# Kernel optimization log

Measured on AMD Instinct MI355X. Metric: run time of the kernel, lower is better.

Reference implementation:

```python
import jax, jax.numpy as jnp
import numpy as np

EPS = 1e-10


def _log_scaling(feats):
    """Raw feats (..., 15): xmin,ymin,xmax,ymax,area,angle,pca_big,pca_small,hu1..hu7
    -> (..., 17): xmin..area, log|pca_big..hu7|, lshape, cosangle, sinangle."""
    lshape = jnp.sqrt(feats[..., 7:8]) / (jnp.sqrt(feats[..., 6:7]) + EPS)
    cosangle = jnp.cos(feats[..., 5:6])
    sinangle = jnp.sin(feats[..., 5:6])
    logged = jnp.log(jnp.abs(feats[..., 5:]) + EPS)  # cols 5..14 logged
    # original drops the (logged) angle column 5 and keeps logged cols 6..14
    return jnp.concatenate([feats[..., :5], logged[..., 1:], lshape, cosangle, sinangle], axis=-1)


def _make_parents(n_trees, P, seed=0):
    """Valid topologically-ordered tree: parent[p] < p, parent[0] = 0 (root)."""
    rng = np.random.default_rng(seed)
    idx = np.arange(P)
    high = np.maximum(idx, 1)
    par = rng.integers(0, 2**31 - 1, size=(n_trees, P)) % high[None, :]
    par[:, 0] = 0
    return par.astype(np.int32)


def setup_inputs() -> dict:
    key = jax.random.key(0)
    k1, k2, k3, k4 = jax.random.split(key, 4)
    B, N, H, W = 2, 2, 1024, 1024
    P = H * W
    x = jax.random.normal(k1, (B, N, H, W), dtype=jnp.float32) * 10.0
    weight = jax.random.uniform(k2, (N, 17, 1), dtype=jnp.float32, minval=-0.01, maxval=0.01)
    bias = jnp.zeros((N, 1), dtype=jnp.float32)
    attrs = jax.random.uniform(k3, (B, N, P, 15), dtype=jnp.float32) * 4.0
    parents = jnp.asarray(_make_parents(B * N, P).reshape(B, N, P))
    return {"x": x, "weight": weight, "bias": bias, "attrs": attrs, "parents": parents}


def _path_sum(contrib_pad, par_pad, P):
    """Pointer-doubling root-to-node path sums over a tree with sentinel at index P."""
    iters = max(int(np.ceil(np.log2(max(P, 2)))), 1)

    def body(i, carry):
        v, p = carry
        return v + v[p], p[p]

    v, _ = jax.lax.fori_loop(0, iters, body, (contrib_pad, par_pad))
    return v[:P]


def reference(x, weight, bias, attrs, parents):
    B, N, H, W = x.shape
    P = H * W
    xf = x.reshape(B, N, P)
    idx = jnp.arange(P, dtype=parents.dtype)
    is_root = parents == idx  # (B,N,P)
    parent_vals = jnp.take_along_axis(xf, parents, axis=-1)
    diff = jnp.where(is_root, xf, xf - parent_vals)  # per-node gray-level increment
    feats = _log_scaling(attrs)  # (B,N,P,17)
    lin = jnp.einsum('bnpf,nfo->bnpo', feats, weight) + bias[None, :, None, :]
    scores = jax.nn.sigmoid(lin[..., 0])  # (B,N,P)
    contrib = diff * scores
    # sentinel node P with contribution 0; roots point at the sentinel
    sent = jnp.full((B, N, 1), P, dtype=parents.dtype)
    par_pad = jnp.concatenate([jnp.where(is_root, P, parents), sent], axis=-1)
    contrib_pad = jnp.concatenate([contrib, jnp.zeros((B, N, 1), x.dtype)], axis=-1)
    out = jax.vmap(jax.vmap(lambda c, p: _path_sum(c, p, P)))(contrib_pad, par_pad)
    return out.reshape(B, N, H, W)
```

## Files before the change

kernel.cpp:

```cpp
#include <hip/hip_runtime.h>
#include <math.h>

#define EPSF 1e-10f
#define P_NODES (1 << 20)
#define T_FRONT 65536
#define T_MID   262144

struct __align__(8) NodePair {
    float v;
    int   par;
};

__global__ __launch_bounds__(256) void score_kernel(
    const float* __restrict__ x,
    const float* __restrict__ weight,
    const float* __restrict__ bias,
    const float* __restrict__ attrs,
    const int*   __restrict__ parents,
    NodePair*    __restrict__ dst,
    int N)
{
    __shared__ float sA[256 * 15];

    const int t = threadIdx.x;
    const int blockBase = blockIdx.x * 256;
    const int idx = blockBase + t;

    const float4* ab4 = (const float4*)(attrs + (size_t)blockBase * 15);
    float4* sA4 = (float4*)sA;
#pragma unroll
    for (int k = t; k < 960; k += 256)
        sA4[k] = ab4[k];

    const int tree = blockBase >> 20;
    const int n    = tree % N;
    const float* w = weight + n * 17;
    const float  b = bias[n];

    __syncthreads();

    const float* a = &sA[t * 15];

    float acc = b;
    acc += a[0] * w[0];
    acc += a[1] * w[1];
    acc += a[2] * w[2];
    acc += a[3] * w[3];
    acc += a[4] * w[4];

    const float a5 = a[5];
    const float a6 = a[6];
    const float a7 = a[7];

    acc += __logf(fabsf(a6)    + EPSF) * w[5];
    acc += __logf(fabsf(a7)    + EPSF) * w[6];
    acc += __logf(fabsf(a[8])  + EPSF) * w[7];
    acc += __logf(fabsf(a[9])  + EPSF) * w[8];
    acc += __logf(fabsf(a[10]) + EPSF) * w[9];
    acc += __logf(fabsf(a[11]) + EPSF) * w[10];
    acc += __logf(fabsf(a[12]) + EPSF) * w[11];
    acc += __logf(fabsf(a[13]) + EPSF) * w[12];
    acc += __logf(fabsf(a[14]) + EPSF) * w[13];

    const float lshape = __fsqrt_rn(a7) / (__fsqrt_rn(a6) + EPSF);
    acc += lshape * w[14];
    acc += __cosf(a5) * w[15];
    acc += __sinf(a5) * w[16];

    const float score = 1.0f / (1.0f + __expf(-acc));

    const int   p   = idx & (P_NODES - 1);
    const int   par = parents[idx];
    const float xv  = x[idx];

    NodePair r;
    if (par == p) {
        r.v   = xv * score;
        r.par = -1;
    } else {
        r.v   = (xv - x[(idx - p) + par]) * score;
        r.par = par;
    }
    dst[idx] = r;
}

__global__ __launch_bounds__(256) void frontier_kernel(
    const NodePair* __restrict__ pairs,
    float*          __restrict__ out)
{
    const int j  = blockIdx.x * blockDim.x + threadIdx.x;
    const int p0 = j * 2;
    if (p0 >= T_FRONT) return;

    const int base = blockIdx.y << 20;
    const NodePair* tp = pairs + base;

    float4 r = *(const float4*)(tp + p0);
    float s0 = r.x;  int c0 = __float_as_int(r.y);
    float s1 = r.z;  int c1 = __float_as_int(r.w);

    while (c0 >= 0 || c1 >= 0) {
        NodePair q0, q1;
        bool a0 = (c0 >= 0), a1 = (c1 >= 0);
        if (a0) q0 = tp[c0];
        if (a1) q1 = tp[c1];
        if (a0) { s0 += q0.v; c0 = q0.par; }
        if (a1) { s1 += q1.v; c1 = q1.par; }
    }

    float2 o; o.x = s0; o.y = s1;
    *(float2*)(out + base + p0) = o;
}

__global__ __launch_bounds__(256) void chunk_kernel(
    const NodePair* __restrict__ pairs,
    float*          __restrict__ out,
    int lo, int hi)
{
    const int j  = blockIdx.x * blockDim.x + threadIdx.x;
    const int p0 = lo + j * 2;
    if (p0 >= hi) return;

    const int base = blockIdx.y << 20;
    const NodePair* tp = pairs + base;

    float4 r = *(const float4*)(tp + p0);
    float s0 = r.x;  int c0 = __float_as_int(r.y);
    float s1 = r.z;  int c1 = __float_as_int(r.w);

    bool a0 = (c0 >= lo), a1 = (c1 >= lo);
    while (a0 || a1) {
        NodePair q0, q1;
        if (a0) q0 = tp[c0];
        if (a1) q1 = tp[c1];
        if (a0) { s0 += q0.v; c0 = q0.par; a0 = (c0 >= lo); }
        if (a1) { s1 += q1.v; c1 = q1.par; a1 = (c1 >= lo); }
    }
    s0 += out[base + c0];
    s1 += out[base + c1];

    float2 o; o.x = s0; o.y = s1;
    *(float2*)(out + base + p0) = o;
}

extern "C" void kernel_launch(void* const* d_in, const int* in_sizes, int n_in,
                              void* d_out, int out_size, void* d_ws, size_t ws_size,
                              hipStream_t stream)
{
    const float* x       = (const float*)d_in[0];
    const float* weight  = (const float*)d_in[1];
    const float* bias    = (const float*)d_in[2];
    const float* attrs   = (const float*)d_in[3];
    const int*   parents = (const int*)d_in[4];
    float*       out     = (float*)d_out;

    const int total  = in_sizes[0];
    const int N      = in_sizes[1] / 17;
    const int nTrees = total >> 20;

    NodePair* pairs = (NodePair*)d_ws;

    const int block = 256;
    const int grid  = (total + block - 1) / block;

    score_kernel<<<grid, block, 0, stream>>>(x, weight, bias, attrs, parents,
                                             pairs, N);

    {
        dim3 g((T_FRONT / 2 + block - 1) / block, nTrees);
        frontier_kernel<<<g, block, 0, stream>>>(pairs, out);
    }
    {
        dim3 g(((T_MID - T_FRONT) / 2 + block - 1) / block, nTrees);
        chunk_kernel<<<g, block, 0, stream>>>(pairs, out, T_FRONT, T_MID);
    }
    {
        dim3 g(((P_NODES - T_MID) / 2 + block - 1) / block, nTrees);
        chunk_kernel<<<g, block, 0, stream>>>(pairs, out, T_MID, P_NODES);
    }
}
```

Measured before the change: 438.6 us.

## Walk four nodes per thread and split path sums into five level chunks

Measured after the change: 458.7 us. 1.05x slower.

```diff
diff --git a/kernel.cpp b/kernel.cpp
--- a/kernel.cpp
+++ b/kernel.cpp
@@ -3,8 +3,11 @@
 
 #define EPSF 1e-10f
 #define P_NODES (1 << 20)
-#define T_FRONT 65536
-#define T_MID   262144
+
+#define L0 16384
+#define L1 65536
+#define L2 262144
+#define L3 524288
 
 struct __align__(8) NodePair {
     float v;
@@ -89,27 +92,34 @@
     float*          __restrict__ out)
 {
     const int j  = blockIdx.x * blockDim.x + threadIdx.x;
-    const int p0 = j * 2;
-    if (p0 >= T_FRONT) return;
+    const int p0 = j * 4;
+    if (p0 >= L0) return;
 
     const int base = blockIdx.y << 20;
     const NodePair* tp = pairs + base;
 
-    float4 r = *(const float4*)(tp + p0);
-    float s0 = r.x;  int c0 = __float_as_int(r.y);
-    float s1 = r.z;  int c1 = __float_as_int(r.w);
-
-    while (c0 >= 0 || c1 >= 0) {
-        NodePair q0, q1;
-        bool a0 = (c0 >= 0), a1 = (c1 >= 0);
+    float4 r0 = *(const float4*)(tp + p0);
+    float4 r1 = *(const float4*)(tp + p0 + 2);
+    float s0 = r0.x;  int c0 = __float_as_int(r0.y);
+    float s1 = r0.z;  int c1 = __float_as_int(r0.w);
+    float s2 = r1.x;  int c2 = __float_as_int(r1.y);
+    float s3 = r1.z;  int c3 = __float_as_int(r1.w);
+
+    bool a0 = c0 >= 0, a1 = c1 >= 0, a2 = c2 >= 0, a3 = c3 >= 0;
+    while (a0 || a1 || a2 || a3) {
+        NodePair q0, q1, q2, q3;
         if (a0) q0 = tp[c0];
         if (a1) q1 = tp[c1];
-        if (a0) { s0 += q0.v; c0 = q0.par; }
-        if (a1) { s1 += q1.v; c1 = q1.par; }
-    }
-
-    float2 o; o.x = s0; o.y = s1;
-    *(float2*)(out + base + p0) = o;
+        if (a2) q2 = tp[c2];
+        if (a3) q3 = tp[c3];
+        if (a0) { s0 += q0.v; c0 = q0.par; a0 = c0 >= 0; }
+        if (a1) { s1 += q1.v; c1 = q1.par; a1 = c1 >= 0; }
+        if (a2) { s2 += q2.v; c2 = q2.par; a2 = c2 >= 0; }
+        if (a3) { s3 += q3.v; c3 = q3.par; a3 = c3 >= 0; }
+    }
+
+    float4 o; o.x = s0; o.y = s1; o.z = s2; o.w = s3;
+    *(float4*)(out + base + p0) = o;
 }
 
 __global__ __launch_bounds__(256) void chunk_kernel(
@@ -118,29 +128,38 @@
     int lo, int hi)
 {
     const int j  = blockIdx.x * blockDim.x + threadIdx.x;
-    const int p0 = lo + j * 2;
+    const int p0 = lo + j * 4;
     if (p0 >= hi) return;
 
     const int base = blockIdx.y << 20;
     const NodePair* tp = pairs + base;
 
-    float4 r = *(const float4*)(tp + p0);
-    float s0 = r.x;  int c0 = __float_as_int(r.y);
-    float s1 = r.z;  int c1 = __float_as_int(r.w);
-
-    bool a0 = (c0 >= lo), a1 = (c1 >= lo);
-    while (a0 || a1) {
-        NodePair q0, q1;
+    float4 r0 = *(const float4*)(tp + p0);
+    float4 r1 = *(const float4*)(tp + p0 + 2);
+    float s0 = r0.x;  int c0 = __float_as_int(r0.y);
+    float s1 = r0.z;  int c1 = __float_as_int(r0.w);
+    float s2 = r1.x;  int c2 = __float_as_int(r1.y);
+    float s3 = r1.z;  int c3 = __float_as_int(r1.w);
+
+    bool a0 = c0 >= lo, a1 = c1 >= lo, a2 = c2 >= lo, a3 = c3 >= lo;
+    while (a0 || a1 || a2 || a3) {
+        NodePair q0, q1, q2, q3;
         if (a0) q0 = tp[c0];
         if (a1) q1 = tp[c1];
-        if (a0) { s0 += q0.v; c0 = q0.par; a0 = (c0 >= lo); }
-        if (a1) { s1 += q1.v; c1 = q1.par; a1 = (c1 >= lo); }
+        if (a2) q2 = tp[c2];
+        if (a3) q3 = tp[c3];
+        if (a0) { s0 += q0.v; c0 = q0.par; a0 = c0 >= lo; }
+        if (a1) { s1 += q1.v; c1 = q1.par; a1 = c1 >= lo; }
+        if (a2) { s2 += q2.v; c2 = q2.par; a2 = c2 >= lo; }
+        if (a3) { s3 += q3.v; c3 = q3.par; a3 = c3 >= lo; }
     }
     s0 += out[base + c0];
     s1 += out[base + c1];
-
-    float2 o; o.x = s0; o.y = s1;
-    *(float2*)(out + base + p0) = o;
+    s2 += out[base + c2];
+    s3 += out[base + c3];
+
+    float4 o; o.x = s0; o.y = s1; o.z = s2; o.w = s3;
+    *(float4*)(out + base + p0) = o;
 }
 
 extern "C" void kernel_launch(void* const* d_in, const int* in_sizes, int n_in,
@@ -167,15 +186,23 @@
                                              pairs, N);
 
     {
-        dim3 g((T_FRONT / 2 + block - 1) / block, nTrees);
+        dim3 g((L0 / 4 + block - 1) / block, nTrees);
         frontier_kernel<<<g, block, 0, stream>>>(pairs, out);
     }
     {
-        dim3 g(((T_MID - T_FRONT) / 2 + block - 1) / block, nTrees);
-        chunk_kernel<<<g, block, 0, stream>>>(pairs, out, T_FRONT, T_MID);
-    }
-    {
-        dim3 g(((P_NODES - T_MID) / 2 + block - 1) / block, nTrees);
-        chunk_kernel<<<g, block, 0, stream>>>(pairs, out, T_MID, P_NODES);
-    }
-}
+        dim3 g(((L1 - L0) / 4 + block - 1) / block, nTrees);
+        chunk_kernel<<<g, block, 0, stream>>>(pairs, out, L0, L1);
+    }
+    {
+        dim3 g(((L2 - L1) / 4 + block - 1) / block, nTrees);
+        chunk_kernel<<<g, block, 0, stream>>>(pairs, out, L1, L2);
+    }
+    {
+        dim3 g(((L3 - L2) / 4 + block - 1) / block, nTrees);
+        chunk_kernel<<<g, block, 0, stream>>>(pairs, out, L2, L3);
+    }
+    {
+        dim3 g(((P_NODES - L3) / 4 + block - 1) / block, nTrees);
+        chunk_kernel<<<g, block, 0, stream>>>(pairs, out, L3, P_NODES);
+    }
+}
```
